# Kernel tuning notes

Measured on AMD Instinct MI355X. Metric: run time of the kernel, lower is better.

Reference implementation:

```python
import jax, jax.numpy as jnp
import numpy as np
import math

DIM = 2048
B, Q_LEN, KV_LEN = 8, 128, 4096


def setup_inputs() -> dict:
    key = jax.random.key(0)
    ks = jax.random.split(key, 8)
    x = jax.random.normal(ks[0], (B, Q_LEN, DIM), dtype=jnp.float32)
    mask = jnp.zeros((B, Q_LEN, KV_LEN + Q_LEN), dtype=bool)  # unused by the original forward
    k_cache = jax.random.normal(ks[1], (B, KV_LEN, DIM), dtype=jnp.float32)
    v_cache = jax.random.normal(ks[2], (B, KV_LEN, DIM), dtype=jnp.float32)
    scale = 1.0 / math.sqrt(DIM)
    wq = jax.random.normal(ks[3], (DIM, DIM), dtype=jnp.float32) * scale
    wk = jax.random.normal(ks[4], (DIM, DIM), dtype=jnp.float32) * scale
    wv = jax.random.normal(ks[5], (DIM, DIM), dtype=jnp.float32) * scale
    wo = jax.random.normal(ks[6], (DIM, DIM), dtype=jnp.float32) * scale
    return {"x": x, "mask": mask, "k_cache": k_cache, "v_cache": v_cache,
            "wq": wq, "wk": wk, "wv": wv, "wo": wo}


def reference(x, mask, k_cache, v_cache, wq, wk, wv, wo):
    # Linear layers (torch: y = x @ W^T)
    q = jnp.einsum('bsd,ed->bse', x, wq)
    k_new = jnp.einsum('bsd,ed->bse', x, wk)
    v_new = jnp.einsum('bsd,ed->bse', x, wv)
    # KV-cache growth via concat (the pattern the kernel replaces)
    k = jnp.concatenate([k_cache, k_new], axis=1)  # [B, KV+Q, D]
    v = jnp.concatenate([v_cache, v_new], axis=1)
    scale = 1.0 / math.sqrt(q.shape[-1])
    scores = jnp.einsum('bqd,bkd->bqk', q, k) * scale  # [B, Q, KV+Q]
    attn = jax.nn.softmax(scores, axis=-1)             # NOTE: mask is unused, as in original
    out = jnp.einsum('bqk,bkd->bqd', attn, v)
    return jnp.einsum('bqd,ed->bqe', out, wo)
```

## Files before the change

kernel.cpp:

```cpp
#include <hip/hip_runtime.h>

typedef __bf16 bf16;
typedef __bf16 bf16x4 __attribute__((ext_vector_type(4)));
typedef __bf16 bf16x8 __attribute__((ext_vector_type(8)));
typedef float f32x4 __attribute__((ext_vector_type(4)));

#define DIM   2048
#define BQ    128
#define KVL   4096
#define KVT   4224
#define M_TOT 1024

__device__ __forceinline__ int swz(int row, int col) {
  return row * 64 + (col ^ ((row & 7) << 3));
}

template<int ROWS, int NTHR>
__device__ __forceinline__ void stage_f32(const float* __restrict__ src, int ld,
                                          bf16* dst, int tid) {
  constexpr int ITERS = (ROWS * 16) / NTHR;
  const int r0 = tid >> 4;
  const int c  = (tid & 15) * 4;
  #pragma unroll
  for (int j = 0; j < ITERS; ++j) {
    int row = j * (NTHR / 16) + r0;
    const float4 v = *reinterpret_cast<const float4*>(src + (size_t)row * ld + c);
    bf16x4 b;
    b[0] = (bf16)v.x; b[1] = (bf16)v.y; b[2] = (bf16)v.z; b[3] = (bf16)v.w;
    *reinterpret_cast<bf16x4*>(dst + swz(row, c)) = b;
  }
}

template<int ROWS, int NTHR>
__device__ __forceinline__ void stage_bf16(const bf16* __restrict__ src, int ld,
                                           bf16* dst, int tid) {
  constexpr int ITERS = (ROWS * 8) / NTHR;
  const int r0 = tid >> 3;
  const int c  = (tid & 7) * 8;
  #pragma unroll
  for (int j = 0; j < ITERS; ++j) {
    int row = j * (NTHR / 8) + r0;
    bf16x8 v = *reinterpret_cast<const bf16x8*>(src + (size_t)row * ld + c);
    *reinterpret_cast<bf16x8*>(dst + swz(row, c)) = v;
  }
}

template<int MF, int NF>
__device__ __forceinline__ void mma_tile(const bf16* As, const bf16* Bs,
                                         f32x4 (&acc)[MF][NF], int l, int wm, int wn) {
  const int ar = l & 15;
  const int ak = (l >> 4) * 8;
  bf16x8 a[MF][2], b[NF][2];
  #pragma unroll
  for (int mi = 0; mi < MF; ++mi)
    #pragma unroll
    for (int kk = 0; kk < 2; ++kk) {
      int row = wm + mi * 16 + ar;
      a[mi][kk] = *reinterpret_cast<const bf16x8*>(As + swz(row, kk * 32 + ak));
    }
  #pragma unroll
  for (int ni = 0; ni < NF; ++ni)
    #pragma unroll
    for (int kk = 0; kk < 2; ++kk) {
      int row = wn + ni * 16 + ar;
      b[ni][kk] = *reinterpret_cast<const bf16x8*>(Bs + swz(row, kk * 32 + ak));
    }
  #pragma unroll
  for (int kk = 0; kk < 2; ++kk)
    #pragma unroll
    for (int mi = 0; mi < MF; ++mi)
      #pragma unroll
      for (int ni = 0; ni < NF; ++ni)
        acc[mi][ni] = __builtin_amdgcn_mfma_f32_16x16x32_bf16(
            a[mi][kk], b[ni][kk], acc[mi][ni], 0, 0, 0);
}

__global__ __launch_bounds__(256) void k_qkv(const float* __restrict__ x,
    const float* __restrict__ wq, const float* __restrict__ wk,
    const float* __restrict__ wv,
    bf16* __restrict__ qb, bf16* __restrict__ kb, bf16* __restrict__ vb) {
  __shared__ bf16 As[128 * 64];
  __shared__ bf16 Bs[64 * 64];
  const int nt = blockIdx.x;
  const int mt = blockIdx.y;
  const int w  = nt >> 5;
  const int nloc = (nt & 31) * 64;
  const float* __restrict__ W = (w == 0) ? wq : (w == 1) ? wk : wv;
  bf16* __restrict__ O = (w == 0) ? qb : (w == 1) ? kb : vb;
  const int m0 = mt * 128;
  const int tid = threadIdx.x;
  const int l = tid & 63, wid = tid >> 6;
  const int wm = (wid >> 1) * 64, wn = (wid & 1) * 32;
  f32x4 acc[4][2] = {};
  for (int kt = 0; kt < DIM / 64; ++kt) {
    const int k0 = kt * 64;
    __syncthreads();
    stage_f32<128, 256>(x + (size_t)m0 * DIM + k0, DIM, As, tid);
    stage_f32<64, 256>(W + (size_t)nloc * DIM + k0, DIM, Bs, tid);
    __syncthreads();
    mma_tile<4, 2>(As, Bs, acc, l, wm, wn);
  }
  const int rr = (l >> 4) * 4, cc = l & 15;
  #pragma unroll
  for (int mi = 0; mi < 4; ++mi)
    #pragma unroll
    for (int ni = 0; ni < 2; ++ni)
      #pragma unroll
      for (int r = 0; r < 4; ++r) {
        int row = m0 + wm + mi * 16 + rr + r;
        int col = nloc + wn + ni * 16 + cc;
        O[(size_t)row * DIM + col] = (bf16)acc[mi][ni][r];
      }
}

__global__ __launch_bounds__(256) void k_scores(const bf16* __restrict__ qb,
    const bf16* __restrict__ kb, const float* __restrict__ kcache,
    float* __restrict__ scores) {
  __shared__ bf16 As[128 * 64];
  __shared__ bf16 Bs[64 * 64];
  const int nt = blockIdx.x;
  const int b  = blockIdx.y;
  const int tid = threadIdx.x;
  const int l = tid & 63, wid = tid >> 6;
  const int wm = (wid >> 1) * 64, wn = (wid & 1) * 32;
  const bf16* Q = qb + (size_t)b * BQ * DIM;
  f32x4 acc[4][2] = {};
  for (int kt = 0; kt < DIM / 64; ++kt) {
    const int k0 = kt * 64;
    __syncthreads();
    stage_bf16<128, 256>(Q + k0, DIM, As, tid);
    if (nt < 64)
      stage_f32<64, 256>(kcache + ((size_t)b * KVL + nt * 64) * DIM + k0, DIM, Bs, tid);
    else
      stage_bf16<64, 256>(kb + ((size_t)b * BQ + (nt - 64) * 64) * DIM + k0, DIM, Bs, tid);
    __syncthreads();
    mma_tile<4, 2>(As, Bs, acc, l, wm, wn);
  }
  const float scale = 0.022097086912079608f;
  const int rr = (l >> 4) * 4, cc = l & 15;
  #pragma unroll
  for (int mi = 0; mi < 4; ++mi)
    #pragma unroll
    for (int ni = 0; ni < 2; ++ni)
      #pragma unroll
      for (int r = 0; r < 4; ++r) {
        int row = wm + mi * 16 + rr + r;
        int col = nt * 64 + wn + ni * 16 + cc;
        scores[((size_t)b * BQ + row) * KVT + col] = acc[mi][ni][r] * scale;
      }
}

__global__ __launch_bounds__(256) void k_softmax(const float* __restrict__ scores,
                                                 bf16* __restrict__ attn) {
  __shared__ float s[KVT];
  __shared__ float red[8];
  const int row = blockIdx.x;
  const int tid = threadIdx.x;
  const size_t base = (size_t)row * KVT;
  float lm = -1e30f;
  for (int i = tid; i < KVT; i += 256) {
    float v = scores[base + i];
    s[i] = v;
    lm = fmaxf(lm, v);
  }
  #pragma unroll
  for (int off = 32; off >= 1; off >>= 1) lm = fmaxf(lm, __shfl_xor(lm, off, 64));
  if ((tid & 63) == 0) red[tid >> 6] = lm;
  __syncthreads();
  const float m = fmaxf(fmaxf(red[0], red[1]), fmaxf(red[2], red[3]));
  float ls = 0.f;
  for (int i = tid; i < KVT; i += 256) {
    float e = __expf(s[i] - m);
    s[i] = e;
    ls += e;
  }
  #pragma unroll
  for (int off = 32; off >= 1; off >>= 1) ls += __shfl_xor(ls, off, 64);
  if ((tid & 63) == 0) red[4 + (tid >> 6)] = ls;
  __syncthreads();
  const float inv = 1.f / (red[4] + red[5] + red[6] + red[7]);
  for (int i = tid; i < KVT; i += 256) attn[base + i] = (bf16)(s[i] * inv);
}

__global__ __launch_bounds__(512) void k_pv(const bf16* __restrict__ attn,
    const float* __restrict__ vcache, const bf16* __restrict__ vb,
    bf16* __restrict__ ob) {
  __shared__ bf16 As[128 * 64];
  __shared__ bf16 VT[64 * 64];
  const int nt = blockIdx.x;
  const int b  = blockIdx.y;
  const int n0 = nt * 64;
  const int tid = threadIdx.x;
  const int l = tid & 63, wid = tid >> 6;
  const int wm = (wid & 3) * 32, wn = (wid >> 2) * 32;
  f32x4 acc[2][2] = {};
  const int vn = tid & 63;
  const int vk = (tid >> 6) * 8;
  for (int kt = 0; kt < KVT / 64; ++kt) {
    const int k0 = kt * 64;
    __syncthreads();
    stage_bf16<128, 512>(attn + (size_t)b * BQ * KVT + k0, KVT, As, tid);
    if (kt < 64) {
      const float* src = vcache + ((size_t)b * KVL + k0) * DIM + n0 + vn;
      #pragma unroll
      for (int j = 0; j < 2; ++j) {
        int kl = vk + j * 4;
        bf16x4 t;
        #pragma unroll
        for (int i = 0; i < 4; ++i) t[i] = (bf16)src[(size_t)(kl + i) * DIM];
        *reinterpret_cast<bf16x4*>(VT + swz(vn, kl)) = t;
      }
    } else {
      const bf16* src = vb + ((size_t)b * BQ + (k0 - KVL)) * DIM + n0 + vn;
      #pragma unroll
      for (int j = 0; j < 2; ++j) {
        int kl = vk + j * 4;
        bf16x4 t;
        #pragma unroll
        for (int i = 0; i < 4; ++i) t[i] = src[(size_t)(kl + i) * DIM];
        *reinterpret_cast<bf16x4*>(VT + swz(vn, kl)) = t;
      }
    }
    __syncthreads();
    mma_tile<2, 2>(As, VT, acc, l, wm, wn);
  }
  const int rr = (l >> 4) * 4, cc = l & 15;
  #pragma unroll
  for (int mi = 0; mi < 2; ++mi)
    #pragma unroll
    for (int ni = 0; ni < 2; ++ni)
      #pragma unroll
      for (int r = 0; r < 4; ++r) {
        int row = wm + mi * 16 + rr + r;
        int col = n0 + wn + ni * 16 + cc;
        ob[((size_t)b * BQ + row) * DIM + col] = (bf16)acc[mi][ni][r];
      }
}

__global__ __launch_bounds__(256) void k_oproj(const bf16* __restrict__ ob,
    const float* __restrict__ wo, float* __restrict__ out) {
  __shared__ bf16 As[64 * 64];
  __shared__ bf16 Bs[64 * 64];
  const int nt = blockIdx.x;
  const int mt = blockIdx.y;
  const int m0 = mt * 64, n0 = nt * 64;
  const int tid = threadIdx.x;
  const int l = tid & 63, wid = tid >> 6;
  const int wm = (wid & 1) * 32, wn = (wid >> 1) * 32;
  f32x4 acc[2][2] = {};
  for (int kt = 0; kt < DIM / 64; ++kt) {
    const int k0 = kt * 64;
    __syncthreads();
    stage_bf16<64, 256>(ob + (size_t)m0 * DIM + k0, DIM, As, tid);
    stage_f32<64, 256>(wo + (size_t)n0 * DIM + k0, DIM, Bs, tid);
    __syncthreads();
    mma_tile<2, 2>(As, Bs, acc, l, wm, wn);
  }
  const int rr = (l >> 4) * 4, cc = l & 15;
  #pragma unroll
  for (int mi = 0; mi < 2; ++mi)
    #pragma unroll
    for (int ni = 0; ni < 2; ++ni)
      #pragma unroll
      for (int r = 0; r < 4; ++r) {
        int row = m0 + wm + mi * 16 + rr + r;
        int col = n0 + wn + ni * 16 + cc;
        out[(size_t)row * DIM + col] = acc[mi][ni][r];
      }
}

extern "C" void kernel_launch(void* const* d_in, const int* in_sizes, int n_in,
                              void* d_out, int out_size, void* d_ws, size_t ws_size,
                              hipStream_t stream) {
  const float* x      = (const float*)d_in[0];
  const float* kcache = (const float*)d_in[2];
  const float* vcache = (const float*)d_in[3];
  const float* wq     = (const float*)d_in[4];
  const float* wk     = (const float*)d_in[5];
  const float* wv     = (const float*)d_in[6];
  const float* wo     = (const float*)d_in[7];
  float* out = (float*)d_out;

  char* ws = (char*)d_ws;
  bf16*  qb     = (bf16*)(ws + 0);
  bf16*  kb     = (bf16*)(ws + 4194304);
  bf16*  vb     = (bf16*)(ws + 8388608);
  float* scores = (float*)(ws + 12582912);
  bf16*  attnb  = (bf16*)(ws + 29884416);
  bf16*  obuf   = (bf16*)(ws + 38535168);

  k_qkv<<<dim3(96, 8), 256, 0, stream>>>(x, wq, wk, wv, qb, kb, vb);
  k_scores<<<dim3(66, 8), 256, 0, stream>>>(qb, kb, kcache, scores);
  k_softmax<<<dim3(1024), 256, 0, stream>>>(scores, attnb);
  k_pv<<<dim3(32, 8), 512, 0, stream>>>(attnb, vcache, vb, obuf);
  k_oproj<<<dim3(32, 16), 256, 0, stream>>>(obuf, wo, out);
}
```

Measured before the change: 288.5 us.

## Double-buffer GEMM staging via register prefetch and enlarge tiles to 512 threads

Every GEMM-style kernel now loads the next K-slice from global memory into registers while the MFMA loop runs on the current shared-memory buffer. The prefetched slice is then written into a second shared buffer, which removes one barrier per iteration. The QKV, scores and output-projection kernels also move to 512-thread blocks with larger 128x128 or 128x64 tiles. This raises data reuse per block and halves the grid sizes. The cost is more registers and shared memory per block, and fewer blocks, which may hurt occupancy or load balance (for example 264 blocks for the scores kernel).

After: 311.9 us. +8.1%, slower.

```diff
diff --git a/kernel.cpp b/kernel.cpp
--- a/kernel.cpp
+++ b/kernel.cpp
@@ -9,41 +9,69 @@
 #define BQ    128
 #define KVL   4096
 #define KVT   4224
-#define M_TOT 1024
 
 __device__ __forceinline__ int swz(int row, int col) {
   return row * 64 + (col ^ ((row & 7) << 3));
 }
 
 template<int ROWS, int NTHR>
-__device__ __forceinline__ void stage_f32(const float* __restrict__ src, int ld,
-                                          bf16* dst, int tid) {
-  constexpr int ITERS = (ROWS * 16) / NTHR;
-  const int r0 = tid >> 4;
-  const int c  = (tid & 15) * 4;
-  #pragma unroll
-  for (int j = 0; j < ITERS; ++j) {
-    int row = j * (NTHR / 16) + r0;
-    const float4 v = *reinterpret_cast<const float4*>(src + (size_t)row * ld + c);
-    bf16x4 b;
-    b[0] = (bf16)v.x; b[1] = (bf16)v.y; b[2] = (bf16)v.z; b[3] = (bf16)v.w;
-    *reinterpret_cast<bf16x4*>(dst + swz(row, c)) = b;
-  }
-}
-
-template<int ROWS, int NTHR>
-__device__ __forceinline__ void stage_bf16(const bf16* __restrict__ src, int ld,
-                                           bf16* dst, int tid) {
-  constexpr int ITERS = (ROWS * 8) / NTHR;
-  const int r0 = tid >> 3;
-  const int c  = (tid & 7) * 8;
-  #pragma unroll
-  for (int j = 0; j < ITERS; ++j) {
-    int row = j * (NTHR / 8) + r0;
-    bf16x8 v = *reinterpret_cast<const bf16x8*>(src + (size_t)row * ld + c);
-    *reinterpret_cast<bf16x8*>(dst + swz(row, c)) = v;
-  }
-}
+struct Stage {
+  static constexpr int NV4 = ROWS * 16 / NTHR;
+  static constexpr int CPT = NV4 * 4;
+  bf16x4 r[NV4];
+  int row, c0;
+  __device__ __forceinline__ void init(int tid) {
+    row = tid / (64 / CPT);
+    c0  = (tid % (64 / CPT)) * CPT;
+  }
+  __device__ __forceinline__ void loadF(const float* __restrict__ src, int ld) {
+    const float* p = src + (size_t)row * ld + c0;
+    #pragma unroll
+    for (int j = 0; j < NV4; ++j) {
+      float4 v = *reinterpret_cast<const float4*>(p + 4 * j);
+      r[j][0] = (bf16)v.x; r[j][1] = (bf16)v.y;
+      r[j][2] = (bf16)v.z; r[j][3] = (bf16)v.w;
+    }
+  }
+  __device__ __forceinline__ void loadB(const bf16* __restrict__ src, int ld) {
+    const bf16* p = src + (size_t)row * ld + c0;
+    #pragma unroll
+    for (int j = 0; j < NV4; j += 2) {
+      bf16x8 v = *reinterpret_cast<const bf16x8*>(p + 4 * j);
+      r[j][0] = v[0]; r[j][1] = v[1]; r[j][2] = v[2]; r[j][3] = v[3];
+      r[j+1][0] = v[4]; r[j+1][1] = v[5]; r[j+1][2] = v[6]; r[j+1][3] = v[7];
+    }
+  }
+  __device__ __forceinline__ void store(bf16* dst) {
+    #pragma unroll
+    for (int j = 0; j < NV4; ++j)
+      *reinterpret_cast<bf16x4*>(dst + swz(row, c0 + 4 * j)) = r[j];
+  }
+};
+
+struct StageVT {
+  bf16x4 r[2];
+  int vn, vk0;
+  __device__ __forceinline__ void init(int tid) { vn = tid & 63; vk0 = (tid >> 6) * 8; }
+  __device__ __forceinline__ void loadF(const float* __restrict__ src) {
+    const float* p = src + (size_t)vk0 * DIM + vn;
+    #pragma unroll
+    for (int j = 0; j < 2; ++j)
+      #pragma unroll
+      for (int i = 0; i < 4; ++i) r[j][i] = (bf16)p[(size_t)(4 * j + i) * DIM];
+  }
+  __device__ __forceinline__ void loadB(const bf16* __restrict__ src) {
+    const bf16* p = src + (size_t)vk0 * DIM + vn;
+    #pragma unroll
+    for (int j = 0; j < 2; ++j)
+      #pragma unroll
+      for (int i = 0; i < 4; ++i) r[j][i] = p[(size_t)(4 * j + i) * DIM];
+  }
+  __device__ __forceinline__ void store(bf16* dst) {
+    *reinterpret_cast<bf16x4*>(dst + swz(vn, vk0))     = r[0];
+    *reinterpret_cast<bf16x4*>(dst + swz(vn, vk0 + 4)) = r[1];
+  }
+};
 
 template<int MF, int NF>
 __device__ __forceinline__ void mma_tile(const bf16* As, const bf16* Bs,
@@ -54,17 +82,13 @@
   #pragma unroll
   for (int mi = 0; mi < MF; ++mi)
     #pragma unroll
-    for (int kk = 0; kk < 2; ++kk) {
-      int row = wm + mi * 16 + ar;
-      a[mi][kk] = *reinterpret_cast<const bf16x8*>(As + swz(row, kk * 32 + ak));
-    }
+    for (int kk = 0; kk < 2; ++kk)
+      a[mi][kk] = *reinterpret_cast<const bf16x8*>(As + swz(wm + mi * 16 + ar, kk * 32 + ak));
   #pragma unroll
   for (int ni = 0; ni < NF; ++ni)
     #pragma unroll
-    for (int kk = 0; kk < 2; ++kk) {
-      int row = wn + ni * 16 + ar;
-      b[ni][kk] = *reinterpret_cast<const bf16x8*>(Bs + swz(row, kk * 32 + ak));
-    }
+    for (int kk = 0; kk < 2; ++kk)
+      b[ni][kk] = *reinterpret_cast<const bf16x8*>(Bs + swz(wn + ni * 16 + ar, kk * 32 + ak));
   #pragma unroll
   for (int kk = 0; kk < 2; ++kk)
     #pragma unroll
@@ -75,30 +99,35 @@
             a[mi][kk], b[ni][kk], acc[mi][ni], 0, 0, 0);
 }
 
-__global__ __launch_bounds__(256) void k_qkv(const float* __restrict__ x,
+__global__ __launch_bounds__(512) void k_qkv(const float* __restrict__ x,
     const float* __restrict__ wq, const float* __restrict__ wk,
     const float* __restrict__ wv,
     bf16* __restrict__ qb, bf16* __restrict__ kb, bf16* __restrict__ vb) {
-  __shared__ bf16 As[128 * 64];
-  __shared__ bf16 Bs[64 * 64];
+  __shared__ bf16 As[2][128 * 64];
+  __shared__ bf16 Bs[2][128 * 64];
   const int nt = blockIdx.x;
-  const int mt = blockIdx.y;
-  const int w  = nt >> 5;
-  const int nloc = (nt & 31) * 64;
+  const int w  = nt >> 4;
+  const int nloc = (nt & 15) * 128;
   const float* __restrict__ W = (w == 0) ? wq : (w == 1) ? wk : wv;
   bf16* __restrict__ O = (w == 0) ? qb : (w == 1) ? kb : vb;
-  const int m0 = mt * 128;
-  const int tid = threadIdx.x;
-  const int l = tid & 63, wid = tid >> 6;
-  const int wm = (wid >> 1) * 64, wn = (wid & 1) * 32;
+  const int m0 = blockIdx.y * 128;
+  const int tid = threadIdx.x, l = tid & 63, wid = tid >> 6;
+  const int wm = (wid >> 2) * 64, wn = (wid & 3) * 32;
+  Stage<128, 512> sa, sb;
+  sa.init(tid); sb.init(tid);
+  const float* Ap = x + (size_t)m0 * DIM;
+  const float* Bp = W + (size_t)nloc * DIM;
   f32x4 acc[4][2] = {};
+  sa.loadF(Ap, DIM); sb.loadF(Bp, DIM);
+  sa.store(As[0]); sb.store(Bs[0]);
+  __syncthreads();
+  int cur = 0;
   for (int kt = 0; kt < DIM / 64; ++kt) {
-    const int k0 = kt * 64;
+    if (kt + 1 < DIM / 64) { sa.loadF(Ap + (kt + 1) * 64, DIM); sb.loadF(Bp + (kt + 1) * 64, DIM); }
+    mma_tile<4, 2>(As[cur], Bs[cur], acc, l, wm, wn);
+    if (kt + 1 < DIM / 64) { sa.store(As[cur ^ 1]); sb.store(Bs[cur ^ 1]); }
     __syncthreads();
-    stage_f32<128, 256>(x + (size_t)m0 * DIM + k0, DIM, As, tid);
-    stage_f32<64, 256>(W + (size_t)nloc * DIM + k0, DIM, Bs, tid);
-    __syncthreads();
-    mma_tile<4, 2>(As, Bs, acc, l, wm, wn);
+    cur ^= 1;
   }
   const int rr = (l >> 4) * 4, cc = l & 15;
   #pragma unroll
@@ -113,28 +142,36 @@
       }
 }
 
-__global__ __launch_bounds__(256) void k_scores(const bf16* __restrict__ qb,
+__global__ __launch_bounds__(512) void k_scores(const bf16* __restrict__ qb,
     const bf16* __restrict__ kb, const float* __restrict__ kcache,
     float* __restrict__ scores) {
-  __shared__ bf16 As[128 * 64];
-  __shared__ bf16 Bs[64 * 64];
+  __shared__ bf16 As[2][128 * 64];
+  __shared__ bf16 Bs[2][128 * 64];
   const int nt = blockIdx.x;
   const int b  = blockIdx.y;
-  const int tid = threadIdx.x;
-  const int l = tid & 63, wid = tid >> 6;
-  const int wm = (wid >> 1) * 64, wn = (wid & 1) * 32;
+  const int tid = threadIdx.x, l = tid & 63, wid = tid >> 6;
+  const int wm = (wid >> 2) * 64, wn = (wid & 3) * 32;
   const bf16* Q = qb + (size_t)b * BQ * DIM;
+  const bool useCache = (nt < 32);
+  const float* Bf = kcache + ((size_t)b * KVL + nt * 128) * DIM;
+  const bf16*  Bb = kb + (size_t)b * BQ * DIM;
+  Stage<128, 512> sa, sb;
+  sa.init(tid); sb.init(tid);
   f32x4 acc[4][2] = {};
+  sa.loadB(Q, DIM);
+  if (useCache) sb.loadF(Bf, DIM); else sb.loadB(Bb, DIM);
+  sa.store(As[0]); sb.store(Bs[0]);
+  __syncthreads();
+  int cur = 0;
   for (int kt = 0; kt < DIM / 64; ++kt) {
-    const int k0 = kt * 64;
+    if (kt + 1 < DIM / 64) {
+      sa.loadB(Q + (kt + 1) * 64, DIM);
+      if (useCache) sb.loadF(Bf + (kt + 1) * 64, DIM); else sb.loadB(Bb + (kt + 1) * 64, DIM);
+    }
+    mma_tile<4, 2>(As[cur], Bs[cur], acc, l, wm, wn);
+    if (kt + 1 < DIM / 64) { sa.store(As[cur ^ 1]); sb.store(Bs[cur ^ 1]); }
     __syncthreads();
-    stage_bf16<128, 256>(Q + k0, DIM, As, tid);
-    if (nt < 64)
-      stage_f32<64, 256>(kcache + ((size_t)b * KVL + nt * 64) * DIM + k0, DIM, Bs, tid);
-    else
-      stage_bf16<64, 256>(kb + ((size_t)b * BQ + (nt - 64) * 64) * DIM + k0, DIM, Bs, tid);
-    __syncthreads();
-    mma_tile<4, 2>(As, Bs, acc, l, wm, wn);
+    cur ^= 1;
   }
   const float scale = 0.022097086912079608f;
   const int rr = (l >> 4) * 4, cc = l & 15;
@@ -145,7 +182,7 @@
       #pragma unroll
       for (int r = 0; r < 4; ++r) {
         int row = wm + mi * 16 + rr + r;
-        int col = nt * 64 + wn + ni * 16 + cc;
+        int col = nt * 128 + wn + ni * 16 + cc;
         scores[((size_t)b * BQ + row) * KVT + col] = acc[mi][ni][r] * scale;
       }
 }
@@ -185,44 +222,32 @@
 __global__ __launch_bounds__(512) void k_pv(const bf16* __restrict__ attn,
     const float* __restrict__ vcache, const bf16* __restrict__ vb,
     bf16* __restrict__ ob) {
-  __shared__ bf16 As[128 * 64];
-  __shared__ bf16 VT[64 * 64];
-  const int nt = blockIdx.x;
+  __shared__ bf16 As[2][128 * 64];
+  __shared__ bf16 VT[2][64 * 64];
+  const int n0 = blockIdx.x * 64;
   const int b  = blockIdx.y;
-  const int n0 = nt * 64;
-  const int tid = threadIdx.x;
-  const int l = tid & 63, wid = tid >> 6;
-  const int wm = (wid & 3) * 32, wn = (wid >> 2) * 32;
+  const int tid = threadIdx.x, l = tid & 63, wid = tid >> 6;
+  const int wm = (wid >> 1) * 32, wn = (wid & 1) * 32;
+  const bf16* Ap = attn + (size_t)b * BQ * KVT;
+  Stage<128, 512> sa; sa.init(tid);
+  StageVT sv; sv.init(tid);
   f32x4 acc[2][2] = {};
-  const int vn = tid & 63;
-  const int vk = (tid >> 6) * 8;
+  sa.loadB(Ap, KVT);
+  sv.loadF(vcache + (size_t)b * KVL * DIM + n0);
+  sa.store(As[0]); sv.store(VT[0]);
+  __syncthreads();
+  int cur = 0;
   for (int kt = 0; kt < KVT / 64; ++kt) {
-    const int k0 = kt * 64;
+    if (kt + 1 < KVT / 64) {
+      const int k1 = (kt + 1) * 64;
+      sa.loadB(Ap + k1, KVT);
+      if (kt + 1 < 64) sv.loadF(vcache + ((size_t)b * KVL + k1) * DIM + n0);
+      else             sv.loadB(vb + ((size_t)b * BQ + (k1 - KVL)) * DIM + n0);
+    }
+    mma_tile<2, 2>(As[cur], VT[cur], acc, l, wm, wn);
+    if (kt + 1 < KVT / 64) { sa.store(As[cur ^ 1]); sv.store(VT[cur ^ 1]); }
     __syncthreads();
-    stage_bf16<128, 512>(attn + (size_t)b * BQ * KVT + k0, KVT, As, tid);
-    if (kt < 64) {
-      const float* src = vcache + ((size_t)b * KVL + k0) * DIM + n0 + vn;
-      #pragma unroll
-      for (int j = 0; j < 2; ++j) {
-        int kl = vk + j * 4;
-        bf16x4 t;
-        #pragma unroll
-        for (int i = 0; i < 4; ++i) t[i] = (bf16)src[(size_t)(kl + i) * DIM];
-        *reinterpret_cast<bf16x4*>(VT + swz(vn, kl)) = t;
-      }
-    } else {
-      const bf16* src = vb + ((size_t)b * BQ + (k0 - KVL)) * DIM + n0 + vn;
-      #pragma unroll
-      for (int j = 0; j < 2; ++j) {
-        int kl = vk + j * 4;
-        bf16x4 t;
-        #pragma unroll
-        for (int i = 0; i < 4; ++i) t[i] = src[(size_t)(kl + i) * DIM];
-        *reinterpret_cast<bf16x4*>(VT + swz(vn, kl)) = t;
-      }
-    }
-    __syncthreads();
-    mma_tile<2, 2>(As, VT, acc, l, wm, wn);
+    cur ^= 1;
   }
   const int rr = (l >> 4) * 4, cc = l & 15;
   #pragma unroll
@@ -237,24 +262,29 @@
       }
 }
 
-__global__ __launch_bounds__(256) void k_oproj(const bf16* __restrict__ ob,
+__global__ __launch_bounds__(512) void k_oproj(const bf16* __restrict__ ob,
     const float* __restrict__ wo, float* __restrict__ out) {
-  __shared__ bf16 As[64 * 64];
-  __shared__ bf16 Bs[64 * 64];
-  const int nt = blockIdx.x;
-  const int mt = blockIdx.y;
-  const int m0 = mt * 64, n0 = nt * 64;
-  const int tid = threadIdx.x;
-  const int l = tid & 63, wid = tid >> 6;
-  const int wm = (wid & 1) * 32, wn = (wid >> 1) * 32;
+  __shared__ bf16 As[2][128 * 64];
+  __shared__ bf16 Bs[2][64 * 64];
+  const int n0 = blockIdx.x * 64;
+  const int m0 = blockIdx.y * 128;
+  const int tid = threadIdx.x, l = tid & 63, wid = tid >> 6;
+  const int wm = (wid >> 1) * 32, wn = (wid & 1) * 32;
+  Stage<128, 512> sa; sa.init(tid);
+  Stage<64, 512>  sb; sb.init(tid);
+  const bf16*  Apb = ob + (size_t)m0 * DIM;
+  const float* Bpf = wo + (size_t)n0 * DIM;
   f32x4 acc[2][2] = {};
+  sa.loadB(Apb, DIM); sb.loadF(Bpf, DIM);
+  sa.store(As[0]); sb.store(Bs[0]);
+  __syncthreads();
+  int cur = 0;
   for (int kt = 0; kt < DIM / 64; ++kt) {
-    const int k0 = kt * 64;
+    if (kt + 1 < DIM / 64) { sa.loadB(Apb + (kt + 1) * 64, DIM); sb.loadF(Bpf + (kt + 1) * 64, DIM); }
+    mma_tile<2, 2>(As[cur], Bs[cur], acc, l, wm, wn);
+    if (kt + 1 < DIM / 64) { sa.store(As[cur ^ 1]); sb.store(Bs[cur ^ 1]); }
     __syncthreads();
-    stage_bf16<64, 256>(ob + (size_t)m0 * DIM + k0, DIM, As, tid);
-    stage_f32<64, 256>(wo + (size_t)n0 * DIM + k0, DIM, Bs, tid);
-    __syncthreads();
-    mma_tile<2, 2>(As, Bs, acc, l, wm, wn);
+    cur ^= 1;
   }
   const int rr = (l >> 4) * 4, cc = l & 15;
   #pragma unroll
@@ -289,9 +319,9 @@
   bf16*  attnb  = (bf16*)(ws + 29884416);
   bf16*  obuf   = (bf16*)(ws + 38535168);
 
-  k_qkv<<<dim3(96, 8), 256, 0, stream>>>(x, wq, wk, wv, qb, kb, vb);
-  k_scores<<<dim3(66, 8), 256, 0, stream>>>(qb, kb, kcache, scores);
+  k_qkv<<<dim3(48, 8), 512, 0, stream>>>(x, wq, wk, wv, qb, kb, vb);
+  k_scores<<<dim3(33, 8), 512, 0, stream>>>(qb, kb, kcache, scores);
   k_softmax<<<dim3(1024), 256, 0, stream>>>(scores, attnb);
   k_pv<<<dim3(32, 8), 512, 0, stream>>>(attnb, vcache, vb, obuf);
-  k_oproj<<<dim3(32, 16), 256, 0, stream>>>(obuf, wo, out);
-}
+  k_oproj<<<dim3(32, 8), 512, 0, stream>>>(obuf, wo, out);
+}
```

## Enlarge GEMM tiles across QKV, scores, PV and out-projection kernels; fold scale into Q

Applied to the files above, without the earlier changes.

The QKV and scores kernels move to 128x128 output tiles per block (4x4 MFMA fragments per wave), halving the grid and doubling reuse of each staged A tile. The attention softmax scale moves from the scores epilogue into the Q projection output. k_pv drops to 256 threads with 4x2 fragments per wave, and k_oproj uses 128-row A tiles. Larger tiles cut redundant global loads and fp32-to-bf16 conversions, at the cost of more registers and fewer blocks. Grids of 384 or 264 blocks may underfill a 256-CU device. Applying the scale before the bf16 rounding of Q also slightly changes numerics.

Measured after the change: 333.5 us. 1.16x slower.

```diff
diff --git a/kernel.cpp b/kernel.cpp
--- a/kernel.cpp
+++ b/kernel.cpp
@@ -9,7 +9,7 @@
 #define BQ    128
 #define KVL   4096
 #define KVT   4224
-#define M_TOT 1024
+#define SCALE 0.022097086912079608f
 
 __device__ __forceinline__ int swz(int row, int col) {
   return row * 64 + (col ^ ((row & 7) << 3));
@@ -45,6 +45,29 @@
   }
 }
 
+__device__ __forceinline__ void stage_vt_f32(const float* __restrict__ src,
+                                             bf16* dst, int tid) {
+  const int vn = tid & 63, vk0 = (tid >> 6) * 16;
+  #pragma unroll
+  for (int j = 0; j < 4; ++j) {
+    bf16x4 t;
+    #pragma unroll
+    for (int i = 0; i < 4; ++i) t[i] = (bf16)src[(size_t)(vk0 + 4 * j + i) * DIM + vn];
+    *reinterpret_cast<bf16x4*>(dst + swz(vn, vk0 + 4 * j)) = t;
+  }
+}
+__device__ __forceinline__ void stage_vt_bf16(const bf16* __restrict__ src,
+                                              bf16* dst, int tid) {
+  const int vn = tid & 63, vk0 = (tid >> 6) * 16;
+  #pragma unroll
+  for (int j = 0; j < 4; ++j) {
+    bf16x4 t;
+    #pragma unroll
+    for (int i = 0; i < 4; ++i) t[i] = src[(size_t)(vk0 + 4 * j + i) * DIM + vn];
+    *reinterpret_cast<bf16x4*>(dst + swz(vn, vk0 + 4 * j)) = t;
+  }
+}
+
 template<int MF, int NF>
 __device__ __forceinline__ void mma_tile(const bf16* As, const bf16* Bs,
                                          f32x4 (&acc)[MF][NF], int l, int wm, int wn) {
@@ -54,17 +77,13 @@
   #pragma unroll
   for (int mi = 0; mi < MF; ++mi)
     #pragma unroll
-    for (int kk = 0; kk < 2; ++kk) {
-      int row = wm + mi * 16 + ar;
-      a[mi][kk] = *reinterpret_cast<const bf16x8*>(As + swz(row, kk * 32 + ak));
-    }
+    for (int kk = 0; kk < 2; ++kk)
+      a[mi][kk] = *reinterpret_cast<const bf16x8*>(As + swz(wm + mi * 16 + ar, kk * 32 + ak));
   #pragma unroll
   for (int ni = 0; ni < NF; ++ni)
     #pragma unroll
-    for (int kk = 0; kk < 2; ++kk) {
-      int row = wn + ni * 16 + ar;
-      b[ni][kk] = *reinterpret_cast<const bf16x8*>(Bs + swz(row, kk * 32 + ak));
-    }
+    for (int kk = 0; kk < 2; ++kk)
+      b[ni][kk] = *reinterpret_cast<const bf16x8*>(Bs + swz(wn + ni * 16 + ar, kk * 32 + ak));
   #pragma unroll
   for (int kk = 0; kk < 2; ++kk)
     #pragma unroll
@@ -80,36 +99,36 @@
     const float* __restrict__ wv,
     bf16* __restrict__ qb, bf16* __restrict__ kb, bf16* __restrict__ vb) {
   __shared__ bf16 As[128 * 64];
-  __shared__ bf16 Bs[64 * 64];
+  __shared__ bf16 Bs[128 * 64];
   const int nt = blockIdx.x;
-  const int mt = blockIdx.y;
-  const int w  = nt >> 5;
-  const int nloc = (nt & 31) * 64;
+  const int w  = nt >> 4;
+  const int nloc = (nt & 15) * 128;
   const float* __restrict__ W = (w == 0) ? wq : (w == 1) ? wk : wv;
   bf16* __restrict__ O = (w == 0) ? qb : (w == 1) ? kb : vb;
-  const int m0 = mt * 128;
-  const int tid = threadIdx.x;
-  const int l = tid & 63, wid = tid >> 6;
-  const int wm = (wid >> 1) * 64, wn = (wid & 1) * 32;
-  f32x4 acc[4][2] = {};
+  const float osc = (w == 0) ? SCALE : 1.0f;
+  const int m0 = blockIdx.y * 128;
+  const int tid = threadIdx.x, l = tid & 63, wid = tid >> 6;
+  const int wm = (wid >> 1) * 64, wn = (wid & 1) * 64;
+  const float* Ap = x + (size_t)m0 * DIM;
+  const float* Bp = W + (size_t)nloc * DIM;
+  f32x4 acc[4][4] = {};
   for (int kt = 0; kt < DIM / 64; ++kt) {
-    const int k0 = kt * 64;
-    __syncthreads();
-    stage_f32<128, 256>(x + (size_t)m0 * DIM + k0, DIM, As, tid);
-    stage_f32<64, 256>(W + (size_t)nloc * DIM + k0, DIM, Bs, tid);
-    __syncthreads();
-    mma_tile<4, 2>(As, Bs, acc, l, wm, wn);
-  }
-  const int rr = (l >> 4) * 4, cc = l & 15;
-  #pragma unroll
-  for (int mi = 0; mi < 4; ++mi)
-    #pragma unroll
-    for (int ni = 0; ni < 2; ++ni)
+    __syncthreads();
+    stage_f32<128, 256>(Ap + kt * 64, DIM, As, tid);
+    stage_f32<128, 256>(Bp + kt * 64, DIM, Bs, tid);
+    __syncthreads();
+    mma_tile<4, 4>(As, Bs, acc, l, wm, wn);
+  }
+  const int rr = (l >> 4) * 4, cc = l & 15;
+  #pragma unroll
+  for (int mi = 0; mi < 4; ++mi)
+    #pragma unroll
+    for (int ni = 0; ni < 4; ++ni)
       #pragma unroll
       for (int r = 0; r < 4; ++r) {
         int row = m0 + wm + mi * 16 + rr + r;
         int col = nloc + wn + ni * 16 + cc;
-        O[(size_t)row * DIM + col] = (bf16)acc[mi][ni][r];
+        O[(size_t)row * DIM + col] = (bf16)(acc[mi][ni][r] * osc);
       }
 }
 
@@ -117,36 +136,35 @@
     const bf16* __restrict__ kb, const float* __restrict__ kcache,
     float* __restrict__ scores) {
   __shared__ bf16 As[128 * 64];
-  __shared__ bf16 Bs[64 * 64];
+  __shared__ bf16 Bs[128 * 64];
   const int nt = blockIdx.x;
   const int b  = blockIdx.y;
-  const int tid = threadIdx.x;
-  const int l = tid & 63, wid = tid >> 6;
-  const int wm = (wid >> 1) * 64, wn = (wid & 1) * 32;
+  const int tid = threadIdx.x, l = tid & 63, wid = tid >> 6;
+  const int wm = (wid >> 1) * 64, wn = (wid & 1) * 64;
   const bf16* Q = qb + (size_t)b * BQ * DIM;
-  f32x4 acc[4][2] = {};
+  const bool useCache = (nt < 32);
+  const float* Bf = kcache + ((size_t)b * KVL + nt * 128) * DIM;
+  const bf16*  Bb = kb + (size_t)b * BQ * DIM;
+  f32x4 acc[4][4] = {};
   for (int kt = 0; kt < DIM / 64; ++kt) {
     const int k0 = kt * 64;
     __syncthreads();
     stage_bf16<128, 256>(Q + k0, DIM, As, tid);
-    if (nt < 64)
-      stage_f32<64, 256>(kcache + ((size_t)b * KVL + nt * 64) * DIM + k0, DIM, Bs, tid);
-    else
-      stage_bf16<64, 256>(kb + ((size_t)b * BQ + (nt - 64) * 64) * DIM + k0, DIM, Bs, tid);
-    __syncthreads();
-    mma_tile<4, 2>(As, Bs, acc, l, wm, wn);
-  }
-  const float scale = 0.022097086912079608f;
-  const int rr = (l >> 4) * 4, cc = l & 15;
-  #pragma unroll
-  for (int mi = 0; mi < 4; ++mi)
-    #pragma unroll
-    for (int ni = 0; ni < 2; ++ni)
+    if (useCache) stage_f32<128, 256>(Bf + k0, DIM, Bs, tid);
+    else          stage_bf16<128, 256>(Bb + k0, DIM, Bs, tid);
+    __syncthreads();
+    mma_tile<4, 4>(As, Bs, acc, l, wm, wn);
+  }
+  const int rr = (l >> 4) * 4, cc = l & 15;
+  #pragma unroll
+  for (int mi = 0; mi < 4; ++mi)
+    #pragma unroll
+    for (int ni = 0; ni < 4; ++ni)
       #pragma unroll
       for (int r = 0; r < 4; ++r) {
         int row = wm + mi * 16 + rr + r;
-        int col = nt * 64 + wn + ni * 16 + cc;
-        scores[((size_t)b * BQ + row) * KVT + col] = acc[mi][ni][r] * scale;
+        int col = nt * 128 + wn + ni * 16 + cc;
+        scores[((size_t)b * BQ + row) * KVT + col] = acc[mi][ni][r];
       }
 }
 
@@ -182,51 +200,29 @@
   for (int i = tid; i < KVT; i += 256) attn[base + i] = (bf16)(s[i] * inv);
 }
 
-__global__ __launch_bounds__(512) void k_pv(const bf16* __restrict__ attn,
+__global__ __launch_bounds__(256) void k_pv(const bf16* __restrict__ attn,
     const float* __restrict__ vcache, const bf16* __restrict__ vb,
     bf16* __restrict__ ob) {
   __shared__ bf16 As[128 * 64];
   __shared__ bf16 VT[64 * 64];
-  const int nt = blockIdx.x;
+  const int n0 = blockIdx.x * 64;
   const int b  = blockIdx.y;
-  const int n0 = nt * 64;
-  const int tid = threadIdx.x;
-  const int l = tid & 63, wid = tid >> 6;
-  const int wm = (wid & 3) * 32, wn = (wid >> 2) * 32;
-  f32x4 acc[2][2] = {};
-  const int vn = tid & 63;
-  const int vk = (tid >> 6) * 8;
+  const int tid = threadIdx.x, l = tid & 63, wid = tid >> 6;
+  const int wm = (wid >> 1) * 64, wn = (wid & 1) * 32;
+  const bf16* Ap = attn + (size_t)b * BQ * KVT;
+  f32x4 acc[4][2] = {};
   for (int kt = 0; kt < KVT / 64; ++kt) {
     const int k0 = kt * 64;
     __syncthreads();
-    stage_bf16<128, 512>(attn + (size_t)b * BQ * KVT + k0, KVT, As, tid);
-    if (kt < 64) {
-      const float* src = vcache + ((size_t)b * KVL + k0) * DIM + n0 + vn;
-      #pragma unroll
-      for (int j = 0; j < 2; ++j) {
-        int kl = vk + j * 4;
-        bf16x4 t;
-        #pragma unroll
-        for (int i = 0; i < 4; ++i) t[i] = (bf16)src[(size_t)(kl + i) * DIM];
-        *reinterpret_cast<bf16x4*>(VT + swz(vn, kl)) = t;
-      }
-    } else {
-      const bf16* src = vb + ((size_t)b * BQ + (k0 - KVL)) * DIM + n0 + vn;
-      #pragma unroll
-      for (int j = 0; j < 2; ++j) {
-        int kl = vk + j * 4;
-        bf16x4 t;
-        #pragma unroll
-        for (int i = 0; i < 4; ++i) t[i] = src[(size_t)(kl + i) * DIM];
-        *reinterpret_cast<bf16x4*>(VT + swz(vn, kl)) = t;
-      }
-    }
-    __syncthreads();
-    mma_tile<2, 2>(As, VT, acc, l, wm, wn);
-  }
-  const int rr = (l >> 4) * 4, cc = l & 15;
-  #pragma unroll
-  for (int mi = 0; mi < 2; ++mi)
+    stage_bf16<128, 256>(Ap + k0, KVT, As, tid);
+    if (kt < 64) stage_vt_f32(vcache + ((size_t)b * KVL + k0) * DIM + n0, VT, tid);
+    else         stage_vt_bf16(vb + ((size_t)b * BQ + (k0 - KVL)) * DIM + n0, VT, tid);
+    __syncthreads();
+    mma_tile<4, 2>(As, VT, acc, l, wm, wn);
+  }
+  const int rr = (l >> 4) * 4, cc = l & 15;
+  #pragma unroll
+  for (int mi = 0; mi < 4; ++mi)
     #pragma unroll
     for (int ni = 0; ni < 2; ++ni)
       #pragma unroll
@@ -239,26 +235,26 @@
 
 __global__ __launch_bounds__(256) void k_oproj(const bf16* __restrict__ ob,
     const float* __restrict__ wo, float* __restrict__ out) {
-  __shared__ bf16 As[64 * 64];
+  __shared__ bf16 As[128 * 64];
   __shared__ bf16 Bs[64 * 64];
-  const int nt = blockIdx.x;
-  const int mt = blockIdx.y;
-  const int m0 = mt * 64, n0 = nt * 64;
-  const int tid = threadIdx.x;
-  const int l = tid & 63, wid = tid >> 6;
-  const int wm = (wid & 1) * 32, wn = (wid >> 1) * 32;
-  f32x4 acc[2][2] = {};
+  const int n0 = blockIdx.x * 64;
+  const int m0 = blockIdx.y * 128;
+  const int tid = threadIdx.x, l = tid & 63, wid = tid >> 6;
+  const int wm = (wid >> 1) * 64, wn = (wid & 1) * 32;
+  const bf16*  Apb = ob + (size_t)m0 * DIM;
+  const float* Bpf = wo + (size_t)n0 * DIM;
+  f32x4 acc[4][2] = {};
   for (int kt = 0; kt < DIM / 64; ++kt) {
     const int k0 = kt * 64;
     __syncthreads();
-    stage_bf16<64, 256>(ob + (size_t)m0 * DIM + k0, DIM, As, tid);
-    stage_f32<64, 256>(wo + (size_t)n0 * DIM + k0, DIM, Bs, tid);
-    __syncthreads();
-    mma_tile<2, 2>(As, Bs, acc, l, wm, wn);
-  }
-  const int rr = (l >> 4) * 4, cc = l & 15;
-  #pragma unroll
-  for (int mi = 0; mi < 2; ++mi)
+    stage_bf16<128, 256>(Apb + k0, DIM, As, tid);
+    stage_f32<64, 256>(Bpf + k0, DIM, Bs, tid);
+    __syncthreads();
+    mma_tile<4, 2>(As, Bs, acc, l, wm, wn);
+  }
+  const int rr = (l >> 4) * 4, cc = l & 15;
+  #pragma unroll
+  for (int mi = 0; mi < 4; ++mi)
     #pragma unroll
     for (int ni = 0; ni < 2; ++ni)
       #pragma unroll
@@ -289,9 +285,9 @@
   bf16*  attnb  = (bf16*)(ws + 29884416);
   bf16*  obuf   = (bf16*)(ws + 38535168);
 
-  k_qkv<<<dim3(96, 8), 256, 0, stream>>>(x, wq, wk, wv, qb, kb, vb);
-  k_scores<<<dim3(66, 8), 256, 0, stream>>>(qb, kb, kcache, scores);
+  k_qkv<<<dim3(48, 8), 256, 0, stream>>>(x, wq, wk, wv, qb, kb, vb);
+  k_scores<<<dim3(33, 8), 256, 0, stream>>>(qb, kb, kcache, scores);
   k_softmax<<<dim3(1024), 256, 0, stream>>>(scores, attnb);
-  k_pv<<<dim3(32, 8), 512, 0, stream>>>(attnb, vcache, vb, obuf);
-  k_oproj<<<dim3(32, 16), 256, 0, stream>>>(obuf, wo, out);
-}
+  k_pv<<<dim3(32, 8), 256, 0, stream>>>(attnb, vcache, vb, obuf);
+  k_oproj<<<dim3(32, 8), 256, 0, stream>>>(obuf, wo, out);
+}
```
